# Performance work log

Hardware: AMD Instinct MI355X
Metric: run time of the kernel (lower is better)

## Reference

```python
import jax, jax.numpy as jnp
import numpy as np

V, E, C, H = 50000, 300, 128, 128
B, SC, SE = 128, 512, 64


def gru_scan(x, lengths, gate_w, gate_b, cand_w, cand_b):
    """TF GRUCell dynamic_rnn: x [B,S,E] -> outputs [B,S,C], zeroed past lengths."""
    Bn, S, _ = x.shape
    Cn = cand_w.shape[1]

    def step(h, inp):
        xt, t = inp  # xt [B,E]
        ru = jax.nn.sigmoid(jnp.concatenate([xt, h], axis=-1) @ gate_w + gate_b)
        r, u = jnp.split(ru, 2, axis=-1)
        c = jnp.tanh(jnp.concatenate([xt, r * h], axis=-1) @ cand_w + cand_b)
        hn = u * h + (1.0 - u) * c
        active = (t < lengths)[:, None]
        hn = jnp.where(active, hn, h)
        out = jnp.where(active, hn, 0.0)
        return hn, out

    h0 = jnp.zeros((Bn, Cn), dtype=x.dtype)
    _, outs = jax.lax.scan(step, h0, (jnp.swapaxes(x, 0, 1), jnp.arange(S)))
    return jnp.swapaxes(outs, 0, 1)


def reverse_seq(x, lengths):
    """tf.reverse_sequence along time for [B,S,D]."""
    S = x.shape[1]
    t = jnp.arange(S)[None, :]
    L = lengths[:, None]
    idx = jnp.where(t < L, L - 1 - t, t)
    return jnp.take_along_axis(x, idx[:, :, None], axis=1)


def attend(states, att_v, att_w, att_b):
    # states [B,S,C]
    scores = jnp.einsum('bsd,d->bs', jnp.tanh(jnp.einsum('bsc,cd->bsd', states, att_w) + att_b), att_v)
    w = jax.nn.softmax(scores, axis=1)
    return jnp.einsum('bsc,bs->bc', states, w)


def extract_features(seq, lengths, embeddings,
                     fw_gate_w, fw_gate_b, fw_cand_w, fw_cand_b,
                     bw_gate_w, bw_gate_b, bw_cand_w, bw_cand_b,
                     att_v, att_w, att_b):
    emb = embeddings[seq]  # [B,S,E]
    fw_states = gru_scan(emb, lengths, fw_gate_w, fw_gate_b, fw_cand_w, fw_cand_b)
    emb_rev = reverse_seq(emb, lengths)
    bw_out = gru_scan(emb_rev, lengths, bw_gate_w, bw_gate_b, bw_cand_w, bw_cand_b)
    bw_states = reverse_seq(bw_out, lengths)
    fw_c = attend(fw_states, att_v, att_w, att_b)
    bw_c = attend(bw_states, att_v, att_w, att_b)
    return jnp.concatenate([fw_c, bw_c], axis=1)


def setup_inputs() -> dict:
    key = jax.random.key(0)
    ks = jax.random.split(key, 20)
    s = 0.05
    context = jax.random.randint(ks[0], (B, SC), 0, V, dtype=jnp.int32)
    end = jax.random.randint(ks[1], (B, SE), 0, V, dtype=jnp.int32)
    context_length = jnp.clip(jax.random.randint(ks[2], (B,), 1, SC + 1), 1, SC).astype(jnp.int32)
    end_length = jnp.clip(jax.random.randint(ks[3], (B,), 1, SE + 1), 1, SE).astype(jnp.int32)
    return {
        'context': context, 'end': end,
        'context_length': context_length, 'end_length': end_length,
        'embeddings': jax.random.normal(ks[4], (V, E), jnp.float32) * s,
        'fw_gate_w': jax.random.normal(ks[5], (E + C, 2 * C), jnp.float32) * s,
        'fw_gate_b': jnp.ones((2 * C,), jnp.float32),
        'fw_cand_w': jax.random.normal(ks[6], (E + C, C), jnp.float32) * s,
        'fw_cand_b': jnp.zeros((C,), jnp.float32),
        'bw_gate_w': jax.random.normal(ks[7], (E + C, 2 * C), jnp.float32) * s,
        'bw_gate_b': jnp.ones((2 * C,), jnp.float32),
        'bw_cand_w': jax.random.normal(ks[8], (E + C, C), jnp.float32) * s,
        'bw_cand_b': jnp.zeros((C,), jnp.float32),
        'att_v': jax.random.normal(ks[9], (C,), jnp.float32) * s,
        'att_w': jax.random.normal(ks[10], (C, C), jnp.float32) * s,
        'att_b': jnp.zeros((C,), jnp.float32),
        'hid_w': jax.random.normal(ks[11], (4 * C, H), jnp.float32) * s,
        'hid_b': jnp.zeros((H,), jnp.float32),
        'out_w': jax.random.normal(ks[12], (H, 1), jnp.float32) * s,
        'out_b': jnp.zeros((1,), jnp.float32),
    }


def reference(context, end, context_length, end_length, embeddings,
              fw_gate_w, fw_gate_b, fw_cand_w, fw_cand_b,
              bw_gate_w, bw_gate_b, bw_cand_w, bw_cand_b,
              att_v, att_w, att_b, hid_w, hid_b, out_w, out_b):
    ctx_f = extract_features(context, context_length, embeddings,
                             fw_gate_w, fw_gate_b, fw_cand_w, fw_cand_b,
                             bw_gate_w, bw_gate_b, bw_cand_w, bw_cand_b,
                             att_v, att_w, att_b)
    end_f = extract_features(end, end_length, embeddings,
                             fw_gate_w, fw_gate_b, fw_cand_w, fw_cand_b,
                             bw_gate_w, bw_gate_b, bw_cand_w, bw_cand_b,
                             att_v, att_w, att_b)
    feats = jnp.concatenate([ctx_f, end_f], axis=1)  # [B, 4C]
    hidden = jax.nn.relu(feats @ hid_w + hid_b)
    logit = (hidden @ out_w + out_b)[:, 0]  # [B]
    return logit
```

## Files before the change

### kernel.cpp

```cpp
#include <hip/hip_runtime.h>
#include <cstdint>
#include <cmath>

static constexpr int V_  = 50000;
static constexpr int E_  = 300;
static constexpr int C_  = 128;
static constexpr int B_  = 128;
static constexpr int SC_ = 512;
static constexpr int SE_ = 64;
static constexpr int NCOL = 768;
static constexpr int KP  = 320;

static constexpr size_t OFF_PROJ  = 0;
static constexpr size_t SZ_PROJ   = (size_t)V_ * NCOL;
static constexpr size_t OFF_WXP   = OFF_PROJ + SZ_PROJ;
static constexpr size_t SZ_WXP    = (size_t)304 * NCOL;
static constexpr size_t OFF_UALL  = OFF_WXP + SZ_WXP;
static constexpr size_t SZ_UALL   = (size_t)C_ * NCOL;
static constexpr size_t OFF_BIAS  = OFF_UALL + SZ_UALL;
static constexpr size_t SZ_BIAS   = NCOL;
static constexpr size_t OFF_ST    = OFF_BIAS + SZ_BIAS;
static constexpr size_t SZ_ST_CTX = (size_t)B_ * SC_ * C_;
static constexpr size_t SZ_ST_END = (size_t)B_ * SE_ * C_;
static constexpr size_t SZ_ST     = 2*SZ_ST_CTX + 2*SZ_ST_END;
static constexpr size_t OFF_FEATS = OFF_ST + SZ_ST;
static constexpr size_t SZ_FEATS  = (size_t)B_ * 512;
static constexpr size_t OFF_BT    = OFF_FEATS + SZ_FEATS;
static constexpr size_t SZ_BT     = (size_t)NCOL * KP / 2 * 2;
static constexpr size_t OFF_AWT   = OFF_BT + SZ_BT;

typedef __attribute__((ext_vector_type(8))) short bf16x8;
typedef __attribute__((ext_vector_type(4))) float f32x4;

static __device__ __forceinline__ unsigned short f2bf_rne(float f) {
  unsigned u = __float_as_uint(f);
  unsigned r = u + 0x7fffu + ((u >> 16) & 1u);
  return (unsigned short)(r >> 16);
}

static __device__ __forceinline__ void gload_lds16(const short* g, short* l) {
  __builtin_amdgcn_global_load_lds(
      (const __attribute__((address_space(1))) void*)g,
      (__attribute__((address_space(3))) void*)l, 16, 0, 0);
}

static __device__ __forceinline__ float fast_sigmoid(float x) {
  return __builtin_amdgcn_rcpf(1.f + __expf(-x));
}
static __device__ __forceinline__ float fast_tanh(float x) {
  return fmaf(-2.f, __builtin_amdgcn_rcpf(__expf(2.f * x) + 1.f), 1.f);
}

__global__ void pack_kernel(const float* __restrict__ fw_gw, const float* __restrict__ fw_gb,
                            const float* __restrict__ fw_cw, const float* __restrict__ fw_cb,
                            const float* __restrict__ bw_gw, const float* __restrict__ bw_gb,
                            const float* __restrict__ bw_cw, const float* __restrict__ bw_cb,
                            float* __restrict__ ws) {
  int i = blockIdx.x * 256 + threadIdx.x;
  float* Wxp  = ws + OFF_WXP;
  float* Uall = ws + OFF_UALL;
  float* bias = ws + OFF_BIAS;
  if (i < 304 * NCOL) {
    int k = i / NCOL, c = i % NCOL;
    float v = 0.f;
    if (k < 300) {
      if (c < 256)      v = fw_gw[k*256 + c];
      else if (c < 384) v = fw_cw[k*128 + (c-256)];
      else if (c < 640) v = bw_gw[k*256 + (c-384)];
      else              v = bw_cw[k*128 + (c-640)];
    }
    Wxp[i] = v;
    return;
  }
  int j = i - 304 * NCOL;
  if (j >= 0 && j < 128 * NCOL) {
    int k = j / NCOL, c = j % NCOL;
    int kk = 300 + k;
    float v;
    if (c < 256)      v = fw_gw[kk*256 + c];
    else if (c < 384) v = fw_cw[kk*128 + (c-256)];
    else if (c < 640) v = bw_gw[kk*256 + (c-384)];
    else              v = bw_cw[kk*128 + (c-640)];
    Uall[j] = v;
    return;
  }
  int m = j - 128 * NCOL;
  if (m >= 0 && m < NCOL) {
    float v;
    if (m < 256)      v = fw_gb[m];
    else if (m < 384) v = fw_cb[m-256];
    else if (m < 640) v = bw_gb[m-384];
    else              v = bw_cb[m-640];
    bias[m] = v;
  }
}

__global__ void pack_bt(const float* __restrict__ Wxp, short* __restrict__ Bthi,
                        short* __restrict__ Btlo, const float* __restrict__ att_w,
                        short* __restrict__ awt_hi, short* __restrict__ awt_lo) {
  int i = blockIdx.x * 256 + threadIdx.x;
  if (i < NCOL * KP) {
    int k = i % KP, n = i / KP;
    float v = (k < 304) ? Wxp[(size_t)k * NCOL + n] : 0.f;
    unsigned short h = f2bf_rne(v);
    float hf = __uint_as_float((unsigned)h << 16);
    unsigned short lo = f2bf_rne(v - hf);
    Bthi[i] = (short)h;
    Btlo[i] = (short)lo;
    return;
  }
  int j = i - NCOL * KP;
  if (j < 128 * 128) {
    int d = j >> 7, c = j & 127;
    float v = att_w[(size_t)c * 128 + d];
    unsigned short h = f2bf_rne(v);
    float hf = __uint_as_float((unsigned)h << 16);
    unsigned short lo = f2bf_rne(v - hf);
    awt_hi[j] = (short)h;
    awt_lo[j] = (short)lo;
  }
}

__global__ void pack_emb(const float* __restrict__ emb, short* __restrict__ Ahi,
                         short* __restrict__ Alo) {
  size_t i = (size_t)blockIdx.x * 256 + threadIdx.x;
  if (i >= (size_t)V_ * KP) return;
  int k = (int)(i % KP);
  size_t row = i / KP;
  float v = (k < E_) ? emb[row * E_ + k] : 0.f;
  unsigned short h = f2bf_rne(v);
  float hf = __uint_as_float((unsigned)h << 16);
  unsigned short lo = f2bf_rne(v - hf);
  Ahi[i] = (short)h;
  Alo[i] = (short)lo;
}

__global__ __launch_bounds__(256) void gemm_mfma(
    const short* __restrict__ Ahi, const short* __restrict__ Alo,
    const short* __restrict__ Bthi, const short* __restrict__ Btlo,
    float* __restrict__ proj) {
  __shared__ short lds[16384];
  int tid = threadIdx.x, wid = tid >> 6, lane = tid & 63;

  int bid = blockIdx.x;
  int xcd = bid & 7, idx = bid >> 3;
  int wgid = (xcd < 2 ? xcd * 294 : 588 + (xcd - 2) * 293) + idx;
  int m0 = (wgid / 6) * 128;
  int n0 = (wgid % 6) * 128;

  f32x4 acc[4][4] = {};

  int lr = lane >> 2, lc = lane & 3;
  int q0 = wid * 2, q1 = q0 + 1;
  int r0 = q0 * 16 + lr, r1 = q1 * 16 + lr;
  int am0 = m0 + r0; if (am0 > V_ - 1) am0 = V_ - 1;
  int am1 = m0 + r1; if (am1 > V_ - 1) am1 = V_ - 1;
  size_t gaOff0 = (size_t)am0 * KP + lc * 8;
  size_t gaOff1 = (size_t)am1 * KP + lc * 8;
  size_t gbOff0 = (size_t)(n0 + r0) * KP + lc * 8;
  size_t gbOff1 = (size_t)(n0 + r1) * KP + lc * 8;

  int quad = lane >> 4;
  int arow = (wid >> 1) * 64 + (lane & 15);
  int brow = (wid & 1) * 64 + (lane & 15);

  for (int k0 = 0; k0 < KP; k0 += 32) {
    gload_lds16(Ahi  + gaOff0 + k0, lds +         q0 * 512);
    gload_lds16(Ahi  + gaOff1 + k0, lds +         q1 * 512);
    gload_lds16(Alo  + gaOff0 + k0, lds +  4096 + q0 * 512);
    gload_lds16(Alo  + gaOff1 + k0, lds +  4096 + q1 * 512);
    gload_lds16(Bthi + gbOff0 + k0, lds +  8192 + q0 * 512);
    gload_lds16(Bthi + gbOff1 + k0, lds +  8192 + q1 * 512);
    gload_lds16(Btlo + gbOff0 + k0, lds + 12288 + q0 * 512);
    gload_lds16(Btlo + gbOff1 + k0, lds + 12288 + q1 * 512);
    __syncthreads();

    bf16x8 ah[4], al[4], bh[4], bl[4];
#pragma unroll
    for (int i = 0; i < 4; ++i) {
      ah[i] = *(bf16x8*)&lds[        (arow + i*16) * 32 + quad * 8];
      al[i] = *(bf16x8*)&lds[ 4096 + (arow + i*16) * 32 + quad * 8];
      bh[i] = *(bf16x8*)&lds[ 8192 + (brow + i*16) * 32 + quad * 8];
      bl[i] = *(bf16x8*)&lds[12288 + (brow + i*16) * 32 + quad * 8];
    }
#pragma unroll
    for (int i = 0; i < 4; ++i)
#pragma unroll
      for (int j = 0; j < 4; ++j) {
        acc[i][j] = __builtin_amdgcn_mfma_f32_16x16x32_bf16(ah[i], bh[j], acc[i][j], 0, 0, 0);
        acc[i][j] = __builtin_amdgcn_mfma_f32_16x16x32_bf16(ah[i], bl[j], acc[i][j], 0, 0, 0);
        acc[i][j] = __builtin_amdgcn_mfma_f32_16x16x32_bf16(al[i], bh[j], acc[i][j], 0, 0, 0);
      }
    __syncthreads();
  }

  int colb = n0 + (wid & 1) * 64 + (lane & 15);
  int rowb = m0 + (wid >> 1) * 64 + quad * 4;
#pragma unroll
  for (int i = 0; i < 4; ++i) {
    int rb = rowb + i * 16;
#pragma unroll
    for (int j = 0; j < 4; ++j) {
      int cc = colb + j * 16;
#pragma unroll
      for (int r = 0; r < 4; ++r) {
        int rr = rb + r;
        if (rr < V_) proj[(size_t)rr * NCOL + cc] = acc[i][j][r];
      }
    }
  }
}

__global__ __attribute__((amdgpu_flat_work_group_size(256, 256),
                          amdgpu_waves_per_eu(2, 2)))
void recur_attn_kernel(
    const int* __restrict__ ctx, const int* __restrict__ endseq,
    const int* __restrict__ ctx_len, const int* __restrict__ end_len,
    const float* __restrict__ proj, const float* __restrict__ Uall,
    const float* __restrict__ bias, float* __restrict__ states,
    const short* __restrict__ awt_hi, const short* __restrict__ awt_lo,
    const float* __restrict__ att_v, const float* __restrict__ att_b,
    float* __restrict__ feats) {
  __shared__ __align__(16) char smraw[18752];
  float* h_s  = (float*)smraw;
  float* rh_s = h_s + 128;
  float* u_s  = rh_s + 128;
  float (*pg)[260] = (float(*)[260])(u_s + 128);
  float (*pc)[132] = (float(*)[132])(pg + 8);
  float (*st_s)[132] = (float(*)[132])smraw;
  short (*ah_s)[132] = (short(*)[132])(smraw + 8448);
  short (*al_s)[132] = (short(*)[132])(smraw + 12672);
  float (*spart)[16] = (float(*)[16])(smraw + 16896);
  float* score_s = (float*)(smraw + 17152);
  float* cm = (float*)(smraw + 17216);
  float* cl = cm + 128;
  float* ca = cl + 128;

  int bid = blockIdx.x;
  int tid = threadIdx.x;
  const int* seq; int S, L, b, dir, featOff; float* stbase;
  if (bid < 256) {
    b = bid >> 1; dir = bid & 1;
    seq = ctx + b * SC_; S = SC_; L = ctx_len[b];
    stbase = states + (dir ? SZ_ST_CTX : 0) + (size_t)b * SC_ * C_;
    featOff = dir * 128;
  } else {
    int q = bid - 256; b = q >> 1; dir = q & 1;
    seq = endseq + b * SE_; S = SE_; L = end_len[b];
    stbase = states + 2*SZ_ST_CTX + (dir ? SZ_ST_END : 0) + (size_t)b * SE_ * C_;
    featOff = 256 + dir * 128;
  }
  int dirOff = dir ? 384 : 0;
  int kg = tid >> 5, jg = tid & 31;

  {
    float wg[16][8];
    float wc[16][4];
#pragma unroll
    for (int kk = 0; kk < 16; ++kk) {
      const float* up = Uall + (size_t)(kg*16 + kk) * NCOL + dirOff;
      float4 w0 = *(const float4*)(up + jg*8);
      float4 w1 = *(const float4*)(up + jg*8 + 4);
      wg[kk][0]=w0.x; wg[kk][1]=w0.y; wg[kk][2]=w0.z; wg[kk][3]=w0.w;
      wg[kk][4]=w1.x; wg[kk][5]=w1.y; wg[kk][6]=w1.z; wg[kk][7]=w1.w;
      float4 wv = *(const float4*)(up + 256 + jg*4);
      wc[kk][0]=wv.x; wc[kk][1]=wv.y; wc[kk][2]=wv.z; wc[kk][3]=wv.w;
    }
    float bias_g = bias[dirOff + tid];
    float bias_c = (tid < 128) ? bias[dirOff + 256 + tid] : 0.f;

    if (tid < 128) h_s[tid] = 0.f;
    __syncthreads();

    int pos0 = dir ? (L - 1) : 0;
    int tok0 = seq[pos0];
    const float* xr0 = proj + (size_t)tok0 * NCOL + dirOff;
    float xg = xr0[tid];
    float xc = (tid < 128) ? xr0[256 + tid] : 0.f;

    for (int t = 0; t < L; ++t) {
      float xg_n = 0.f, xc_n = 0.f;
      if (t + 1 < L) {
        int pos_n = dir ? (L - 2 - t) : (t + 1);
        int tok_n = seq[pos_n];
        const float* xr = proj + (size_t)tok_n * NCOL + dirOff;
        xg_n = xr[tid];
        xc_n = (tid < 128) ? xr[256 + tid] : 0.f;
      }

      float a[8] = {0.f,0.f,0.f,0.f,0.f,0.f,0.f,0.f};
      const float4* h4 = (const float4*)h_s;
#pragma unroll
      for (int q = 0; q < 4; ++q) {
        float4 hv = h4[kg*4 + q];
        float he[4] = {hv.x, hv.y, hv.z, hv.w};
#pragma unroll
        for (int e = 0; e < 4; ++e)
#pragma unroll
          for (int jj = 0; jj < 8; ++jj)
            a[jj] += he[e] * wg[q*4 + e][jj];
      }
      *(float4*)(&pg[kg][jg*8])     = make_float4(a[0], a[1], a[2], a[3]);
      *(float4*)(&pg[kg][jg*8 + 4]) = make_float4(a[4], a[5], a[6], a[7]);
      __syncthreads();

      float g = xg + bias_g;
#pragma unroll
      for (int k2 = 0; k2 < 8; ++k2) g += pg[k2][tid];
      g = fast_sigmoid(g);

      float h_old = 0.f;
      if (tid < 128) { h_old = h_s[tid]; rh_s[tid] = g * h_old; }
      else           { u_s[tid - 128] = g; }
      __syncthreads();

      float ac[4] = {0.f, 0.f, 0.f, 0.f};
      const float4* rh4 = (const float4*)rh_s;
#pragma unroll
      for (int q = 0; q < 4; ++q) {
        float4 rv = rh4[kg*4 + q];
        float re[4] = {rv.x, rv.y, rv.z, rv.w};
#pragma unroll
        for (int e = 0; e < 4; ++e)
#pragma unroll
          for (int jj = 0; jj < 4; ++jj)
            ac[jj] += re[e] * wc[q*4 + e][jj];
      }
      *(float4*)(&pc[kg][jg*4]) = make_float4(ac[0], ac[1], ac[2], ac[3]);
      __syncthreads();

      if (tid < 128) {
        float cs = xc + bias_c;
#pragma unroll
        for (int k2 = 0; k2 < 8; ++k2) cs += pc[k2][tid];
        float c = fast_tanh(cs);
        float u = u_s[tid];
        float hn = u * h_old + (1.f - u) * c;
        h_s[tid] = hn;
        int pos = dir ? (L - 1 - t) : t;
        stbase[(size_t)pos * C_ + tid] = hn;
      }
      __syncthreads();
      xg = xg_n; xc = xc_n;
    }

    for (int i = L * C_ + tid; i < S * C_; i += 256) stbase[i] = 0.f;
  }
  __syncthreads();

  const float* stb = stbase;
  int w = tid >> 6, lane = tid & 63;
  int quad = lane >> 4, l15 = lane & 15;

  int d0 = 32 * w + l15, d1 = d0 + 16;
  bf16x8 bh0[4], bh1[4], bl0[4], bl1[4];
#pragma unroll
  for (int kt = 0; kt < 4; ++kt) {
    bh0[kt] = *(const bf16x8*)&awt_hi[d0*128 + kt*32 + quad*8];
    bh1[kt] = *(const bf16x8*)&awt_hi[d1*128 + kt*32 + quad*8];
    bl0[kt] = *(const bf16x8*)&awt_lo[d0*128 + kt*32 + quad*8];
    bl1[kt] = *(const bf16x8*)&awt_lo[d1*128 + kt*32 + quad*8];
  }
  float vv0 = att_v[d0], vv1 = att_v[d1];
  float bb0 = att_b[d0], bb1 = att_b[d1];

  int c = tid & 127, half = tid >> 7;
  float m = -1e30f, lsum = 0.f, acc = 0.f;

  int lrow = tid >> 4, lcol = (tid & 15) * 8;
  float4 p0, p1;
  {
    const float* src = stb + (size_t)lrow * C_ + lcol;
    p0 = *(const float4*)(src);
    p1 = *(const float4*)(src + 4);
  }

  int nchunks = S >> 4;
  for (int ch = 0; ch < nchunks; ++ch) {
    __syncthreads();
    float f[8] = {p0.x, p0.y, p0.z, p0.w, p1.x, p1.y, p1.z, p1.w};
    short hi8[8], lo8[8];
#pragma unroll
    for (int j = 0; j < 8; ++j) {
      unsigned short h = f2bf_rne(f[j]);
      float hf = __uint_as_float((unsigned)h << 16);
      hi8[j] = (short)h;
      lo8[j] = (short)f2bf_rne(f[j] - hf);
    }
    *(float4*)(&st_s[lrow][lcol])     = p0;
    *(float4*)(&st_s[lrow][lcol + 4]) = p1;
    *(bf16x8*)(&ah_s[lrow][lcol]) = *(bf16x8*)hi8;
    *(bf16x8*)(&al_s[lrow][lcol]) = *(bf16x8*)lo8;
    if (ch + 1 < nchunks) {
      const float* src = stb + (size_t)((ch + 1) * 16 + lrow) * C_ + lcol;
      p0 = *(const float4*)(src);
      p1 = *(const float4*)(src + 4);
    }
    __syncthreads();

    f32x4 ac0 = {0.f, 0.f, 0.f, 0.f}, ac1 = {0.f, 0.f, 0.f, 0.f};
#pragma unroll
    for (int kt = 0; kt < 4; ++kt) {
      bf16x8 a_hi = *(bf16x8*)&ah_s[l15][kt*32 + quad*8];
      bf16x8 a_lo = *(bf16x8*)&al_s[l15][kt*32 + quad*8];
      ac0 = __builtin_amdgcn_mfma_f32_16x16x32_bf16(a_hi, bh0[kt], ac0, 0, 0, 0);
      ac0 = __builtin_amdgcn_mfma_f32_16x16x32_bf16(a_hi, bl0[kt], ac0, 0, 0, 0);
      ac0 = __builtin_amdgcn_mfma_f32_16x16x32_bf16(a_lo, bh0[kt], ac0, 0, 0, 0);
      ac1 = __builtin_amdgcn_mfma_f32_16x16x32_bf16(a_hi, bh1[kt], ac1, 0, 0, 0);
      ac1 = __builtin_amdgcn_mfma_f32_16x16x32_bf16(a_hi, bl1[kt], ac1, 0, 0, 0);
      ac1 = __builtin_amdgcn_mfma_f32_16x16x32_bf16(a_lo, bh1[kt], ac1, 0, 0, 0);
    }

    float part[4];
#pragma unroll
    for (int r = 0; r < 4; ++r)
      part[r] = fast_tanh(ac0[r] + bb0) * vv0 + fast_tanh(ac1[r] + bb1) * vv1;
#pragma unroll
    for (int mask = 1; mask <= 8; mask <<= 1)
#pragma unroll
      for (int r = 0; r < 4; ++r)
        part[r] += __shfl_xor(part[r], mask, 64);
    if (l15 == 0) {
#pragma unroll
      for (int r = 0; r < 4; ++r) spart[w][quad*4 + r] = part[r];
    }
    __syncthreads();
    if (tid < 16)
      score_s[tid] = spart[0][tid] + spart[1][tid] + spart[2][tid] + spart[3][tid];
    __syncthreads();

    float srow[8]; float smax = m;
#pragma unroll
    for (int r = 0; r < 8; ++r) { srow[r] = score_s[half*8 + r]; smax = fmaxf(smax, srow[r]); }
    float scale = __expf(m - smax);
    acc *= scale; lsum *= scale; m = smax;
#pragma unroll
    for (int r = 0; r < 8; ++r) {
      float wgt = __expf(srow[r] - m);
      lsum += wgt;
      acc += wgt * st_s[half*8 + r][c];
    }
  }

  __syncthreads();
  if (half == 1) { cm[c] = m; cl[c] = lsum; ca[c] = acc; }
  __syncthreads();
  if (half == 0) {
    float m1 = cm[c], l1 = cl[c], a1 = ca[c];
    float M = fmaxf(m, m1);
    float w0 = __expf(m - M), w1 = __expf(m1 - M);
    feats[b * 512 + featOff + c] = (acc * w0 + a1 * w1) / (lsum * w0 + l1 * w1);
  }
}

__global__ __launch_bounds__(128) void head_kernel(
    const float* __restrict__ feats, const float* __restrict__ hid_w,
    const float* __restrict__ hid_b, const float* __restrict__ out_w,
    const float* __restrict__ out_b, float* __restrict__ out) {
  __shared__ __align__(16) float f_s[512];
  __shared__ float part[2];
  int b = blockIdx.x, tid = threadIdx.x;
  for (int i = tid; i < 512; i += 128) f_s[i] = feats[b * 512 + i];
  __syncthreads();
  float h = hid_b[tid];
  for (int k = 0; k < 512; ++k) h += f_s[k] * hid_w[k * 128 + tid];
  h = fmaxf(h, 0.f);
  float p = h * out_w[tid];
#pragma unroll
  for (int off = 32; off > 0; off >>= 1) p += __shfl_xor(p, off, 64);
  if ((tid & 63) == 0) part[tid >> 6] = p;
  __syncthreads();
  if (tid == 0) out[b] = part[0] + part[1] + out_b[0];
}

extern "C" void kernel_launch(void* const* d_in, const int* in_sizes, int n_in,
                              void* d_out, int out_size, void* d_ws, size_t ws_size,
                              hipStream_t stream) {
  const int*   ctx     = (const int*)d_in[0];
  const int*   endseq  = (const int*)d_in[1];
  const int*   ctx_len = (const int*)d_in[2];
  const int*   end_len = (const int*)d_in[3];
  const float* emb     = (const float*)d_in[4];
  const float* fw_gw   = (const float*)d_in[5];
  const float* fw_gb   = (const float*)d_in[6];
  const float* fw_cw   = (const float*)d_in[7];
  const float* fw_cb   = (const float*)d_in[8];
  const float* bw_gw   = (const float*)d_in[9];
  const float* bw_gb   = (const float*)d_in[10];
  const float* bw_cw   = (const float*)d_in[11];
  const float* bw_cb   = (const float*)d_in[12];
  const float* att_v   = (const float*)d_in[13];
  const float* att_w   = (const float*)d_in[14];
  const float* att_b   = (const float*)d_in[15];
  const float* hid_w   = (const float*)d_in[16];
  const float* hid_b   = (const float*)d_in[17];
  const float* out_w   = (const float*)d_in[18];
  const float* out_b   = (const float*)d_in[19];
  float* ws  = (float*)d_ws;
  float* out = (float*)d_out;

  short* Ahi    = (short*)(ws + OFF_ST);
  short* Alo    = Ahi + (size_t)V_ * KP;
  short* Bthi   = (short*)(ws + OFF_BT);
  short* Btlo   = Bthi + (size_t)NCOL * KP;
  short* awt_hi = (short*)(ws + OFF_AWT);
  short* awt_lo = awt_hi + 128 * 128;

  pack_kernel<<<1299, 256, 0, stream>>>(fw_gw, fw_gb, fw_cw, fw_cb,
                                        bw_gw, bw_gb, bw_cw, bw_cb, ws);
  pack_bt<<<(NCOL * KP + 128 * 128 + 255) / 256, 256, 0, stream>>>(
      ws + OFF_WXP, Bthi, Btlo, att_w, awt_hi, awt_lo);
  pack_emb<<<(int)(((size_t)V_ * KP + 255) / 256), 256, 0, stream>>>(emb, Ahi, Alo);

  gemm_mfma<<<2346, 256, 0, stream>>>(Ahi, Alo, Bthi, Btlo, ws + OFF_PROJ);

  recur_attn_kernel<<<512, 256, 0, stream>>>(ctx, endseq, ctx_len, end_len,
                                             ws + OFF_PROJ, ws + OFF_UALL,
                                             ws + OFF_BIAS, ws + OFF_ST,
                                             awt_hi, awt_lo, att_v, att_b,
                                             ws + OFF_FEATS);

  head_kernel<<<128, 128, 0, stream>>>(ws + OFF_FEATS, hid_w, hid_b,
                                       out_w, out_b, out);
}
```

Baseline: 768.4 us.

## Split context-chain attention into separate kernel parallelized over sequence halves

Blocks 0-255 of the fused recurrence kernel, which handle the long context sequences, now return right after the GRU scan instead of running attention. A new attn_kernel handles context attention with two blocks per chain, each covering half the 512 timesteps, and writes online-softmax partials (max, sum, accumulator). The head kernel merges the partials. This is meant to shorten the serial attention tail on the critical path of the long-sequence blocks. The cost is an extra launch and a reread of the states from global memory.

```diff
diff --git a/kernel.cpp b/kernel.cpp
--- a/kernel.cpp
+++ b/kernel.cpp
@@ -213,7 +213,7 @@
 
 __global__ __attribute__((amdgpu_flat_work_group_size(256, 256),
                           amdgpu_waves_per_eu(2, 2)))
-void recur_attn_kernel(
+void recur_fused_kernel(
     const int* __restrict__ ctx, const int* __restrict__ endseq,
     const int* __restrict__ ctx_len, const int* __restrict__ end_len,
     const float* __restrict__ proj, const float* __restrict__ Uall,
@@ -348,6 +348,8 @@
   }
   __syncthreads();
 
+  if (bid < 256) return;
+
   const float* stb = stbase;
   int w = tid >> 6, lane = tid & 63;
   int quad = lane >> 4, l15 = lane & 15;
@@ -453,14 +455,150 @@
   }
 }
 
+__global__ __launch_bounds__(256, 3) void attn_kernel(
+    const float* __restrict__ states, const short* __restrict__ awt_hi,
+    const short* __restrict__ awt_lo, const float* __restrict__ att_v,
+    const float* __restrict__ att_b, float* __restrict__ partials) {
+  __shared__ __align__(16) float st_s[16][132];
+  __shared__ __align__(16) short ah_s[16][132];
+  __shared__ __align__(16) short al_s[16][132];
+  __shared__ float spart[4][16];
+  __shared__ float score_s[16];
+  __shared__ float cm[128], cl[128], ca[128];
+
+  int bid = blockIdx.x, tid = threadIdx.x;
+  int chain = bid >> 1, ph = bid & 1;
+  int b = chain >> 1, dir = chain & 1;
+  const float* stb = states + (dir ? SZ_ST_CTX : 0) + (size_t)b * SC_ * C_;
+  int ch0 = ph * 16, ch1 = ch0 + 16;
+
+  int w = tid >> 6, lane = tid & 63;
+  int quad = lane >> 4, l15 = lane & 15;
+
+  int d0 = 32 * w + l15, d1 = d0 + 16;
+  bf16x8 bh0[4], bh1[4], bl0[4], bl1[4];
+#pragma unroll
+  for (int kt = 0; kt < 4; ++kt) {
+    bh0[kt] = *(const bf16x8*)&awt_hi[d0*128 + kt*32 + quad*8];
+    bh1[kt] = *(const bf16x8*)&awt_hi[d1*128 + kt*32 + quad*8];
+    bl0[kt] = *(const bf16x8*)&awt_lo[d0*128 + kt*32 + quad*8];
+    bl1[kt] = *(const bf16x8*)&awt_lo[d1*128 + kt*32 + quad*8];
+  }
+  float vv0 = att_v[d0], vv1 = att_v[d1];
+  float bb0 = att_b[d0], bb1 = att_b[d1];
+
+  int c = tid & 127, half = tid >> 7;
+  float m = -1e30f, lsum = 0.f, acc = 0.f;
+
+  int lrow = tid >> 4, lcol = (tid & 15) * 8;
+  float4 p0, p1;
+  {
+    const float* src = stb + (size_t)(ch0 * 16 + lrow) * C_ + lcol;
+    p0 = *(const float4*)(src);
+    p1 = *(const float4*)(src + 4);
+  }
+
+  for (int ch = ch0; ch < ch1; ++ch) {
+    __syncthreads();
+    float f[8] = {p0.x, p0.y, p0.z, p0.w, p1.x, p1.y, p1.z, p1.w};
+    short hi8[8], lo8[8];
+#pragma unroll
+    for (int j = 0; j < 8; ++j) {
+      unsigned short h = f2bf_rne(f[j]);
+      float hf = __uint_as_float((unsigned)h << 16);
+      hi8[j] = (short)h;
+      lo8[j] = (short)f2bf_rne(f[j] - hf);
+    }
+    *(float4*)(&st_s[lrow][lcol])     = p0;
+    *(float4*)(&st_s[lrow][lcol + 4]) = p1;
+    *(bf16x8*)(&ah_s[lrow][lcol]) = *(bf16x8*)hi8;
+    *(bf16x8*)(&al_s[lrow][lcol]) = *(bf16x8*)lo8;
+    if (ch + 1 < ch1) {
+      const float* src = stb + (size_t)((ch + 1) * 16 + lrow) * C_ + lcol;
+      p0 = *(const float4*)(src);
+      p1 = *(const float4*)(src + 4);
+    }
+    __syncthreads();
+
+    f32x4 ac0 = {0.f, 0.f, 0.f, 0.f}, ac1 = {0.f, 0.f, 0.f, 0.f};
+#pragma unroll
+    for (int kt = 0; kt < 4; ++kt) {
+      bf16x8 a_hi = *(bf16x8*)&ah_s[l15][kt*32 + quad*8];
+      bf16x8 a_lo = *(bf16x8*)&al_s[l15][kt*32 + quad*8];
+      ac0 = __builtin_amdgcn_mfma_f32_16x16x32_bf16(a_hi, bh0[kt], ac0, 0, 0, 0);
+      ac0 = __builtin_amdgcn_mfma_f32_16x16x32_bf16(a_hi, bl0[kt], ac0, 0, 0, 0);
+      ac0 = __builtin_amdgcn_mfma_f32_16x16x32_bf16(a_lo, bh0[kt], ac0, 0, 0, 0);
+      ac1 = __builtin_amdgcn_mfma_f32_16x16x32_bf16(a_hi, bh1[kt], ac1, 0, 0, 0);
+      ac1 = __builtin_amdgcn_mfma_f32_16x16x32_bf16(a_hi, bl1[kt], ac1, 0, 0, 0);
+      ac1 = __builtin_amdgcn_mfma_f32_16x16x32_bf16(a_lo, bh1[kt], ac1, 0, 0, 0);
+    }
+
+    float part[4];
+#pragma unroll
+    for (int r = 0; r < 4; ++r)
+      part[r] = fast_tanh(ac0[r] + bb0) * vv0 + fast_tanh(ac1[r] + bb1) * vv1;
+#pragma unroll
+    for (int mask = 1; mask <= 8; mask <<= 1)
+#pragma unroll
+      for (int r = 0; r < 4; ++r)
+        part[r] += __shfl_xor(part[r], mask, 64);
+    if (l15 == 0) {
+#pragma unroll
+      for (int r = 0; r < 4; ++r) spart[w][quad*4 + r] = part[r];
+    }
+    __syncthreads();
+    if (tid < 16)
+      score_s[tid] = spart[0][tid] + spart[1][tid] + spart[2][tid] + spart[3][tid];
+    __syncthreads();
+
+    float srow[8]; float smax = m;
+#pragma unroll
+    for (int r = 0; r < 8; ++r) { srow[r] = score_s[half*8 + r]; smax = fmaxf(smax, srow[r]); }
+    float scale = __expf(m - smax);
+    acc *= scale; lsum *= scale; m = smax;
+#pragma unroll
+    for (int r = 0; r < 8; ++r) {
+      float wgt = __expf(srow[r] - m);
+      lsum += wgt;
+      acc += wgt * st_s[half*8 + r][c];
+    }
+  }
+
+  __syncthreads();
+  if (half == 1) { cm[c] = m; cl[c] = lsum; ca[c] = acc; }
+  __syncthreads();
+  if (half == 0) {
+    float m1 = cm[c], l1 = cl[c], a1 = ca[c];
+    float M = fmaxf(m, m1);
+    float w0 = __expf(m - M), w1 = __expf(m1 - M);
+    float Lt = lsum * w0 + l1 * w1;
+    float At = acc * w0 + a1 * w1;
+    float* p = partials + ((size_t)chain * 2 + ph) * 130;
+    if (c == 0) { p[0] = M; p[1] = Lt; }
+    p[2 + c] = At;
+  }
+}
+
 __global__ __launch_bounds__(128) void head_kernel(
-    const float* __restrict__ feats, const float* __restrict__ hid_w,
-    const float* __restrict__ hid_b, const float* __restrict__ out_w,
-    const float* __restrict__ out_b, float* __restrict__ out) {
+    const float* __restrict__ partials, const float* __restrict__ feats,
+    const float* __restrict__ hid_w, const float* __restrict__ hid_b,
+    const float* __restrict__ out_w, const float* __restrict__ out_b,
+    float* __restrict__ out) {
   __shared__ __align__(16) float f_s[512];
   __shared__ float part[2];
   int b = blockIdx.x, tid = threadIdx.x;
-  for (int i = tid; i < 512; i += 128) f_s[i] = feats[b * 512 + i];
+#pragma unroll
+  for (int dir = 0; dir < 2; ++dir) {
+    const float* p0 = partials + ((size_t)(b * 2 + dir) * 2) * 130;
+    const float* p1 = p0 + 130;
+    float m0 = p0[0], l0 = p0[1], a0 = p0[2 + tid];
+    float m1 = p1[0], l1 = p1[1], a1 = p1[2 + tid];
+    float M = fmaxf(m0, m1);
+    float w0 = __expf(m0 - M), w1 = __expf(m1 - M);
+    f_s[dir * 128 + tid] = (a0 * w0 + a1 * w1) / (l0 * w0 + l1 * w1);
+  }
+  f_s[256 + tid] = feats[b * 512 + 256 + tid];
+  f_s[384 + tid] = feats[b * 512 + 384 + tid];
   __syncthreads();
   float h = hid_b[tid];
   for (int k = 0; k < 512; ++k) h += f_s[k] * hid_w[k * 128 + tid];
@@ -505,6 +643,7 @@
   short* Btlo   = Bthi + (size_t)NCOL * KP;
   short* awt_hi = (short*)(ws + OFF_AWT);
   short* awt_lo = awt_hi + 128 * 128;
+  float* partials = ws + OFF_BT;
 
   pack_kernel<<<1299, 256, 0, stream>>>(fw_gw, fw_gb, fw_cw, fw_cb,
                                         bw_gw, bw_gb, bw_cw, bw_cb, ws);
@@ -514,12 +653,15 @@
 
   gemm_mfma<<<2346, 256, 0, stream>>>(Ahi, Alo, Bthi, Btlo, ws + OFF_PROJ);
 
-  recur_attn_kernel<<<512, 256, 0, stream>>>(ctx, endseq, ctx_len, end_len,
-                                             ws + OFF_PROJ, ws + OFF_UALL,
-                                             ws + OFF_BIAS, ws + OFF_ST,
-                                             awt_hi, awt_lo, att_v, att_b,
-                                             ws + OFF_FEATS);
-
-  head_kernel<<<128, 128, 0, stream>>>(ws + OFF_FEATS, hid_w, hid_b,
-                                       out_w, out_b, out);
-}
+  recur_fused_kernel<<<512, 256, 0, stream>>>(ctx, endseq, ctx_len, end_len,
+                                              ws + OFF_PROJ, ws + OFF_UALL,
+                                              ws + OFF_BIAS, ws + OFF_ST,
+                                              awt_hi, awt_lo, att_v, att_b,
+                                              ws + OFF_FEATS);
+
+  attn_kernel<<<512, 256, 0, stream>>>(ws + OFF_ST, awt_hi, awt_lo,
+                                       att_v, att_b, partials);
+
+  head_kernel<<<128, 128, 0, stream>>>(partials, ws + OFF_FEATS,
+                                       hid_w, hid_b, out_w, out_b, out);
+}
```

Result: no change. 754.5 us (-1.8%).
